# Kernel optimization log

Measured on AMD Instinct MI355X. Metric: run time of the kernel, lower is better.

## Reference

```python
import jax, jax.numpy as jnp
import numpy as np

EPS = 1e-5

def conv1x1(x, w, b):
    # x: [B,C,H,W], w: [O,C], b: [O]
    return jnp.einsum('bchw,oc->bohw', x, w) + b[None, :, None, None]

def bn(x, g, be, m, v):
    inv = g / jnp.sqrt(v + EPS)
    return x * inv[None, :, None, None] + (be - m * inv)[None, :, None, None]

def mrconv4d(x, w, b, g, be, m, v, K):
    B, C, H, W = x.shape
    x_j = jnp.zeros_like(x)
    # torch.cat([x[:,:,-i:,:], x[:,:,:-i,:]], dim=2) == roll by +i along H
    for i in range(K, H, K):
        x_j = jnp.maximum(x_j, x - jnp.roll(x, i, axis=2))
    for i in range(K, W, K):
        x_j = jnp.maximum(x_j, x - jnp.roll(x, i, axis=3))
    y = jnp.concatenate([x, x_j], axis=1)  # [B,2C,H,W]
    y = conv1x1(y, w, b)
    y = bn(y, g, be, m, v)
    return jax.nn.gelu(y, approximate=False)

def setup_inputs() -> dict:
    key = jax.random.key(0)
    ks = jax.random.split(key, 20)
    B, C, H, W = 16, 384, 56, 56
    C2 = 2 * C
    d = {}
    d['x'] = jax.random.normal(ks[0], (B, C, H, W), dtype=jnp.float32)
    d['fc1_w'] = jax.random.normal(ks[1], (C, C), dtype=jnp.float32) * 0.02
    d['fc1_b'] = jax.random.normal(ks[2], (C,), dtype=jnp.float32) * 0.02
    d['fc1_g'] = jax.random.uniform(ks[3], (C,), dtype=jnp.float32) + 0.5
    d['fc1_be'] = jax.random.normal(ks[4], (C,), dtype=jnp.float32) * 0.02
    d['fc1_m'] = jax.random.normal(ks[5], (C,), dtype=jnp.float32) * 0.02
    d['fc1_v'] = jax.random.uniform(ks[6], (C,), dtype=jnp.float32) + 0.5
    d['gc_w'] = jax.random.normal(ks[7], (C2, C2), dtype=jnp.float32) * 0.02
    d['gc_b'] = jax.random.normal(ks[8], (C2,), dtype=jnp.float32) * 0.02
    d['gc_g'] = jax.random.uniform(ks[9], (C2,), dtype=jnp.float32) + 0.5
    d['gc_be'] = jax.random.normal(ks[10], (C2,), dtype=jnp.float32) * 0.02
    d['gc_m'] = jax.random.normal(ks[11], (C2,), dtype=jnp.float32) * 0.02
    d['gc_v'] = jax.random.uniform(ks[12], (C2,), dtype=jnp.float32) + 0.5
    d['fc2_w'] = jax.random.normal(ks[13], (C, C2), dtype=jnp.float32) * 0.02
    d['fc2_b'] = jax.random.normal(ks[14], (C,), dtype=jnp.float32) * 0.02
    d['fc2_g'] = jax.random.uniform(ks[15], (C,), dtype=jnp.float32) + 0.5
    d['fc2_be'] = jax.random.normal(ks[16], (C,), dtype=jnp.float32) * 0.02
    d['fc2_m'] = jax.random.normal(ks[17], (C,), dtype=jnp.float32) * 0.02
    d['fc2_v'] = jax.random.uniform(ks[18], (C,), dtype=jnp.float32) + 0.5
    d['K'] = 2
    return d

def reference(x, fc1_w, fc1_b, fc1_g, fc1_be, fc1_m, fc1_v,
              gc_w, gc_b, gc_g, gc_be, gc_m, gc_v,
              fc2_w, fc2_b, fc2_g, fc2_be, fc2_m, fc2_v, K):
    res = x
    h = bn(conv1x1(x, fc1_w, fc1_b), fc1_g, fc1_be, fc1_m, fc1_v)
    h = mrconv4d(h, gc_w, gc_b, gc_g, gc_be, gc_m, gc_v, K)
    h = bn(conv1x1(h, fc2_w, fc2_b), fc2_g, fc2_be, fc2_m, fc2_v)
    return h + res  # drop_path=0 -> identity
```

## Files before the change

### kernel.cpp

```cpp
#include <hip/hip_runtime.h>

#define P_ 3136
#define NTOT 50176
#define EPSV 1e-5f

typedef __bf16 bf16x8 __attribute__((ext_vector_type(8)));
typedef float f32x4 __attribute__((ext_vector_type(4)));
typedef unsigned short u16x8 __attribute__((ext_vector_type(8)));
typedef unsigned short u16x4 __attribute__((ext_vector_type(4)));

__device__ __forceinline__ unsigned short f2bf(float f) {
    unsigned u = __builtin_bit_cast(unsigned, f);
    unsigned r = u + 0x7fffu + ((u >> 16) & 1u);
    return (unsigned short)(r >> 16);
}
__device__ __forceinline__ float bf2f(unsigned short h) {
    unsigned u = ((unsigned)h) << 16;
    return __builtin_bit_cast(float, u);
}

#if __has_builtin(__builtin_amdgcn_cvt_pk_fp8_f32) && __has_builtin(__builtin_amdgcn_cvt_f32_fp8)
#define FP8_HW 1
#else
#define FP8_HW 0
#endif

__device__ __forceinline__ unsigned f2e4m3_sw(float f) {
    unsigned u = __builtin_bit_cast(unsigned, f);
    unsigned s = (u >> 24) & 0x80u;
    float a = fabsf(f);
    if (a >= 448.f) return s | 0x7Eu;
    if (a < 0.015625f) {
        int m = (int)(a * 512.f + 0.5f);
        return s | (unsigned)m;
    }
    unsigned au = __builtin_bit_cast(unsigned, a);
    unsigned r = au + 0x7FFFFu + ((au >> 20) & 1u);
    unsigned e = (r >> 23) - 120u;
    return s | (e << 3) | ((r >> 20) & 7u);
}
__device__ __forceinline__ float e4m3f_sw(unsigned b) {
    unsigned em = b & 0x7fu;
    float v;
    if (em < 8u) v = (float)em * 0.001953125f;
    else v = __builtin_bit_cast(float, (((em >> 3) + 120u) << 23) | ((em & 7u) << 20));
    return (b & 0x80u) ? -v : v;
}
__device__ __forceinline__ unsigned f2e4m3x4(float v0, float v1, float v2, float v3) {
#if FP8_HW
    unsigned pk = (unsigned)__builtin_amdgcn_cvt_pk_fp8_f32(v0, v1, 0, false);
    pk = (unsigned)__builtin_amdgcn_cvt_pk_fp8_f32(v2, v3, (int)pk, true);
    return pk;
#else
    return f2e4m3_sw(v0) | (f2e4m3_sw(v1) << 8) | (f2e4m3_sw(v2) << 16) | (f2e4m3_sw(v3) << 24);
#endif
}
__device__ __forceinline__ unsigned f2e4m3_1(float v) {
#if FP8_HW
    return (unsigned)__builtin_amdgcn_cvt_pk_fp8_f32(v, 0.f, 0, false) & 0xFFu;
#else
    return f2e4m3_sw(v);
#endif
}
__device__ __forceinline__ float e4m3f(unsigned b) {
#if FP8_HW
    return __builtin_amdgcn_cvt_f32_fp8((int)b, 0);
#else
    return e4m3f_sw(b);
#endif
}

__device__ __forceinline__ float gelu_fast(float x) {
    float x2 = x * x;
    float u2 = x * (1.5957691216f + 0.0713548162f * x2);
    u2 = fminf(u2, 80.0f);
    float e = __expf(u2);
    return x * e * __builtin_amdgcn_rcpf(e + 1.0f);
}
__device__ __forceinline__ void gload16(const void* g, void* l) {
    __builtin_amdgcn_global_load_lds(
        (const __attribute__((address_space(1))) void*)g,
        (__attribute__((address_space(3))) void*)l, 16, 0, 0);
}
__device__ __forceinline__ bf16x8 ldlds(const char* p) {
    return __builtin_bit_cast(bf16x8, *(const u16x8*)p);
}

__global__ __launch_bounds__(256)
void prep_wb(const float* __restrict__ w1, const float* __restrict__ w2,
             const float* __restrict__ w3,
             unsigned short* __restrict__ o1, unsigned char* __restrict__ o2q,
             unsigned char* __restrict__ o3q,
             const float* b1, const float* g1, const float* be1, const float* m1, const float* v1,
             const float* b2, const float* g2, const float* be2, const float* m2, const float* v2,
             const float* b3, const float* g3, const float* be3, const float* m3, const float* v3,
             float* bn1, float* bn2, float* bn3)
{
    int i = blockIdx.x * 256 + threadIdx.x;
    const int n1 = 384 * 384 / 4, n2 = 768 * 768 / 4, n3 = 384 * 768 / 4;
    if (i < n1) {
        float4 f = *(const float4*)(w1 + (size_t)i * 4);
        u16x4 pk = { f2bf(f.x), f2bf(f.y), f2bf(f.z), f2bf(f.w) };
        *(u16x4*)(o1 + (size_t)i * 4) = pk;
    } else if (i < n1 + n2) {
        int j = i - n1;
        float4 f = *(const float4*)(w2 + (size_t)j * 4);
        *(unsigned*)(o2q + (size_t)j * 4) =
            f2e4m3x4(f.x * 32.f, f.y * 32.f, f.z * 32.f, f.w * 32.f);
    } else if (i < n1 + n2 + n3) {
        int j = i - n1 - n2;
        float4 f = *(const float4*)(w3 + (size_t)j * 4);
        *(unsigned*)(o3q + (size_t)j * 4) =
            f2e4m3x4(f.x * 32.f, f.y * 32.f, f.z * 32.f, f.w * 32.f);
    } else {
        int k = i - (n1 + n2 + n3);
        const float *pb, *pg, *pbe, *pm, *pv; float* dst; int o, M; float isc = 1.f;
        if (k < 384)       { pb=b1; pg=g1; pbe=be1; pm=m1; pv=v1; dst=bn1; o=k;      M=384; }
        else if (k < 1152) { pb=b2; pg=g2; pbe=be2; pm=m2; pv=v2; dst=bn2; o=k-384;  M=768; isc = 1.f/32.f; }
        else               { pb=b3; pg=g3; pbe=be3; pm=m3; pv=v3; dst=bn3; o=k-1152; M=384; isc = 1.f/256.f; }
        float inv = pg[o] / sqrtf(pv[o] + EPSV);
        dst[o]     = inv * isc;
        dst[M + o] = (pb[o] - pm[o]) * inv + pbe[o];
    }
}

__global__ __launch_bounds__(256)
void prep_xT(const float* __restrict__ x, unsigned short* __restrict__ xT)
{
    __shared__ float tl[64][65];
    const int t = threadIdx.x;
    const int c0 = blockIdx.x * 64;
    const int p0 = blockIdx.y * 64;
    const int b  = blockIdx.z;
    const float* xb = x + ((size_t)b * 384 + c0) * P_ + p0;
    {
        int c = t >> 2, j0 = (t & 3) * 16;
        #pragma unroll
        for (int j = 0; j < 16; j += 4) {
            float4 f4 = *(const float4*)(xb + (size_t)c * P_ + j0 + j);
            tl[c][j0 + j]     = f4.x; tl[c][j0 + j + 1] = f4.y;
            tl[c][j0 + j + 2] = f4.z; tl[c][j0 + j + 3] = f4.w;
        }
    }
    __syncthreads();
    {
        int p = t >> 2, c1 = (t & 3) * 16;
        unsigned short buf[16];
        #pragma unroll
        for (int j = 0; j < 16; ++j) buf[j] = f2bf(tl[c1 + j][p]);
        unsigned short* dst = xT + ((size_t)b * P_ + p0 + p) * 384 + c0 + c1;
        *(u16x8*)dst       = *(u16x8*)buf;
        *(u16x8*)(dst + 8) = *(u16x8*)(buf + 8);
    }
}

__global__ __launch_bounds__(256, 2)
void gemm1(const unsigned short* __restrict__ W, const unsigned short* __restrict__ In,
           unsigned char* __restrict__ Out, const float* __restrict__ bnp)
{
    constexpr int KD = 384, MDIM = 384, NT = KD / 64, MT = MDIM / 128;
    __shared__ __align__(16) char lds[65536];

    const int t    = threadIdx.x;
    const int lane = t & 63;
    const int wave = t >> 6;
    const int wm = wave >> 1, wn = wave & 1;
    const int fr = lane & 15, fg = lane >> 4;

    const int nwg = gridDim.x;
    int id = blockIdx.x;
    int q = nwg >> 3, r = nwg & 7;
    int xcd = id & 7, pos = id >> 3;
    int wg = (xcd < r ? xcd * (q + 1) : r * (q + 1) + (xcd - r) * q) + pos;
    const int m0 = (wg % MT) * 128;
    const int n0 = (wg / MT) * 128;

    const int pcu  = (((t & 7) ^ ((t >> 3) & 7)) << 3);
    const int srow = t >> 3;
    const unsigned short* pA[4];
    const unsigned short* pB[4];
    #pragma unroll
    for (int i = 0; i < 4; ++i) {
        pA[i] = W  + (size_t)(m0 + i * 32 + srow) * KD + pcu;
        pB[i] = In + (size_t)(n0 + i * 32 + srow) * KD + pcu;
    }
    auto stage = [&](int kt) {
        int kk = kt * 64;
        char* base = lds + (kt & 1) * 32768 + t * 16;
        #pragma unroll
        for (int i = 0; i < 4; ++i) gload16(pA[i] + kk, base + i * 4096);
        #pragma unroll
        for (int i = 0; i < 4; ++i) gload16(pB[i] + kk, base + 16384 + i * 4096);
    };

    const int ko0 = (fg * 16) ^ ((fr & 7) << 4);
    const int ko1 = (64 + fg * 16) ^ ((fr & 7) << 4);
    const int arow = wm * 64 + fr;
    const int brow = wn * 64 + fr;

    f32x4 acc[4][4] = {};

    stage(0);

    for (int kt = 0; kt < NT; ++kt) {
        asm volatile("s_waitcnt vmcnt(0)" ::: "memory");
        __builtin_amdgcn_s_barrier();
        __builtin_amdgcn_sched_barrier(0);
        if (kt + 1 < NT) stage(kt + 1);
        __builtin_amdgcn_sched_barrier(0);

        const char* base = lds + (kt & 1) * 32768;
        bf16x8 afr[4][2], bfr[4][2];
        #pragma unroll
        for (int mf = 0; mf < 4; ++mf) {
            afr[mf][0] = ldlds(base + (arow + mf * 16) * 128 + ko0);
            afr[mf][1] = ldlds(base + (arow + mf * 16) * 128 + ko1);
        }
        #pragma unroll
        for (int nf = 0; nf < 4; ++nf) {
            bfr[nf][0] = ldlds(base + 16384 + (brow + nf * 16) * 128 + ko0);
            bfr[nf][1] = ldlds(base + 16384 + (brow + nf * 16) * 128 + ko1);
        }
        #pragma unroll
        for (int ks = 0; ks < 2; ++ks)
            #pragma unroll
            for (int mf = 0; mf < 4; ++mf)
                #pragma unroll
                for (int nf = 0; nf < 4; ++nf)
                    acc[mf][nf] = __builtin_amdgcn_mfma_f32_16x16x32_bf16(
                        afr[mf][ks], bfr[nf][ks], acc[mf][nf], 0, 0, 0);
    }

    asm volatile("s_waitcnt vmcnt(0)" ::: "memory");
    __builtin_amdgcn_s_barrier();

    unsigned char* eL = (unsigned char*)lds;
    #pragma unroll
    for (int mf = 0; mf < 4; ++mf) {
        const int o_l = wm * 64 + mf * 16 + fg * 4;
        f32x4 inv = *(const f32x4*)(bnp + m0 + o_l);
        f32x4 sh  = *(const f32x4*)(bnp + MDIM + m0 + o_l);
        #pragma unroll
        for (int nf = 0; nf < 4; ++nf) {
            const int col_l = wn * 64 + nf * 16 + fr;
            *(unsigned*)(eL + col_l * 144 + o_l) = f2e4m3x4(
                acc[mf][nf][0] * inv[0] + sh[0],
                acc[mf][nf][1] * inv[1] + sh[1],
                acc[mf][nf][2] * inv[2] + sh[2],
                acc[mf][nf][3] * inv[3] + sh[3]);
        }
    }
    __builtin_amdgcn_s_barrier();
    #pragma unroll
    for (int it = 0; it < 8; ++it) {
        const int idx = it * 256 + t;
        const int col = idx >> 4, seg = idx & 15;
        *(unsigned long long*)(Out + (size_t)(n0 + col) * 768 + m0 + seg * 8) =
            *(const unsigned long long*)(eL + col * 144 + seg * 8);
    }
}

template<int MDIM, int EPI>
__device__ __forceinline__ void gemmq_body(
    const unsigned char* __restrict__ W,
    const unsigned char* __restrict__ In,
    void* __restrict__ OutV,
    const float* __restrict__ bnp,
    const float* __restrict__ res,
    char* lds)
{
    constexpr int NT = 6;
    constexpr int MT = MDIM / 128;

    const int t    = threadIdx.x;
    const int lane = t & 63;
    const int wave = t >> 6;
    const int wm = wave >> 1, wn = wave & 1;
    const int fr = lane & 15, fg = lane >> 4;

    const int nwg = gridDim.x;
    int id = blockIdx.x;
    int q = nwg >> 3, r = nwg & 7;
    int xcd = id & 7, pos = id >> 3;
    int wg = (xcd < r ? xcd * (q + 1) : r * (q + 1) + (xcd - r) * q) + pos;
    const int m0 = (wg % MT) * 128;
    const int n0 = (wg / MT) * 128;

    const int pcu  = (((t & 7) ^ ((t >> 3) & 7)) << 4);
    const int srow = t >> 3;
    const unsigned char* pA[4];
    const unsigned char* pB[4];
    #pragma unroll
    for (int i = 0; i < 4; ++i) {
        pA[i] = W  + (size_t)(m0 + i * 32 + srow) * 768 + pcu;
        pB[i] = In + (size_t)(n0 + i * 32 + srow) * 768 + pcu;
    }
    auto stage = [&](int kt) {
        int kk = kt * 128;
        char* base = lds + (kt & 1) * 32768 + t * 16;
        #pragma unroll
        for (int i = 0; i < 4; ++i) gload16(pA[i] + kk, base + i * 4096);
        #pragma unroll
        for (int i = 0; i < 4; ++i) gload16(pB[i] + kk, base + 16384 + i * 4096);
    };

    const int ko0 = (fg * 16) ^ ((fr & 7) << 4);
    const int ko1 = (64 + fg * 16) ^ ((fr & 7) << 4);
    const int arow = wm * 64 + fr;
    const int brow = wn * 64 + fr;

    f32x4 acc[4][4] = {};

    stage(0);

    for (int kt = 0; kt < NT; ++kt) {
        asm volatile("s_waitcnt vmcnt(0)" ::: "memory");
        __builtin_amdgcn_s_barrier();
        __builtin_amdgcn_sched_barrier(0);
        if (kt + 1 < NT) stage(kt + 1);
        __builtin_amdgcn_sched_barrier(0);

        const char* base = lds + (kt & 1) * 32768;
        ulonglong2 afr[4][2], bfr[4][2];
        #pragma unroll
        for (int mf = 0; mf < 4; ++mf) {
            afr[mf][0] = *(const ulonglong2*)(base + (arow + mf * 16) * 128 + ko0);
            afr[mf][1] = *(const ulonglong2*)(base + (arow + mf * 16) * 128 + ko1);
        }
        #pragma unroll
        for (int nf = 0; nf < 4; ++nf) {
            bfr[nf][0] = *(const ulonglong2*)(base + 16384 + (brow + nf * 16) * 128 + ko0);
            bfr[nf][1] = *(const ulonglong2*)(base + 16384 + (brow + nf * 16) * 128 + ko1);
        }
        #pragma unroll
        for (int rd = 0; rd < 2; ++rd)
            #pragma unroll
            for (int hf = 0; hf < 2; ++hf)
                #pragma unroll
                for (int mf = 0; mf < 4; ++mf)
                    #pragma unroll
                    for (int nf = 0; nf < 4; ++nf)
                        acc[mf][nf] = __builtin_amdgcn_mfma_f32_16x16x32_fp8_fp8(
                            (long)(hf ? afr[mf][rd].y : afr[mf][rd].x),
                            (long)(hf ? bfr[nf][rd].y : bfr[nf][rd].x),
                            acc[mf][nf], 0, 0, 0);
    }

    asm volatile("s_waitcnt vmcnt(0)" ::: "memory");
    __builtin_amdgcn_s_barrier();

    if (EPI == 1) {
        unsigned char* eL = (unsigned char*)lds;
        unsigned char* Out = (unsigned char*)OutV;
        #pragma unroll
        for (int mf = 0; mf < 4; ++mf) {
            const int o_l = wm * 64 + mf * 16 + fg * 4;
            f32x4 inv = *(const f32x4*)(bnp + m0 + o_l);
            f32x4 sh  = *(const f32x4*)(bnp + MDIM + m0 + o_l);
            #pragma unroll
            for (int nf = 0; nf < 4; ++nf) {
                const int col_l = wn * 64 + nf * 16 + fr;
                *(unsigned*)(eL + col_l * 144 + o_l) = f2e4m3x4(
                    gelu_fast(acc[mf][nf][0] * inv[0] + sh[0]) * 8.f,
                    gelu_fast(acc[mf][nf][1] * inv[1] + sh[1]) * 8.f,
                    gelu_fast(acc[mf][nf][2] * inv[2] + sh[2]) * 8.f,
                    gelu_fast(acc[mf][nf][3] * inv[3] + sh[3]) * 8.f);
            }
        }
        __builtin_amdgcn_s_barrier();
        #pragma unroll
        for (int it = 0; it < 8; ++it) {
            const int idx = it * 256 + t;
            const int col = idx >> 4, seg = idx & 15;
            *(unsigned long long*)(Out + (size_t)(n0 + col) * 768 + m0 + seg * 8) =
                *(const unsigned long long*)(eL + col * 144 + seg * 8);
        }
    } else {
        float* eL = (float*)lds;
        float* Out = (float*)OutV;
        #pragma unroll
        for (int mf = 0; mf < 4; ++mf) {
            const int o_l = wm * 64 + mf * 16 + fg * 4;
            f32x4 inv = *(const f32x4*)(bnp + m0 + o_l);
            f32x4 sh  = *(const f32x4*)(bnp + MDIM + m0 + o_l);
            #pragma unroll
            for (int nf = 0; nf < 4; ++nf) {
                const int col_l = wn * 64 + nf * 16 + fr;
                #pragma unroll
                for (int rr = 0; rr < 4; ++rr)
                    eL[(o_l + rr) * 128 + col_l] = acc[mf][nf][rr] * inv[rr] + sh[rr];
            }
        }
        __builtin_amdgcn_s_barrier();
        const int b0 = n0 / P_;
        const int r0 = n0 - b0 * P_;
        #pragma unroll
        for (int g8 = 0; g8 < 8; ++g8) {
            size_t adr[8]; float ev[8], rv[8];
            #pragma unroll
            for (int u = 0; u < 8; ++u) {
                const int idx = (g8 * 8 + u) * 256 + t;
                const int o_i = idx >> 7, col = idx & 127;
                int p = r0 + col;
                const int wrap = p >= P_;
                p -= wrap ? P_ : 0;
                adr[u] = (size_t)(b0 + wrap) * 384 * P_ + (size_t)(m0 + o_i) * P_ + p;
                ev[u]  = eL[o_i * 128 + col];
                rv[u]  = res[adr[u]];
            }
            #pragma unroll
            for (int u = 0; u < 8; ++u)
                Out[adr[u]] = ev[u] + rv[u];
        }
    }
}

__global__ __launch_bounds__(256, 2)
void gemm2q(const unsigned char* __restrict__ W, const unsigned char* __restrict__ In,
            void* __restrict__ OutV, const float* __restrict__ bnp)
{
    __shared__ __align__(16) char lds[65536];
    gemmq_body<768, 1>(W, In, OutV, bnp, nullptr, lds);
}
__global__ __launch_bounds__(256, 2)
void gemm3q(const unsigned char* __restrict__ W, const unsigned char* __restrict__ In,
            void* __restrict__ OutV, const float* __restrict__ bnp,
            const float* __restrict__ res)
{
    __shared__ __align__(16) char lds[65536];
    gemmq_body<384, 2>(W, In, OutV, bnp, res, lds);
}

#define MINSEG (16 * 2 * 56 * 384)
__global__ __launch_bounds__(384)
void mr_min(const unsigned char* __restrict__ y, float* __restrict__ mins)
{
    const int c = threadIdx.x;
    const int q = blockIdx.x;
    const int b = blockIdx.y;
    const unsigned char* yb = y + (size_t)b * P_ * 768;
    float m1e = 3.4e38f, m2e = 3.4e38f, m1o = 3.4e38f, m2o = 3.4e38f;
    if (q < 56) {
        int w = q;
        for (int h = 0; h < 56; h += 2) {
            float v0 = e4m3f(yb[(size_t)(h * 56 + w) * 768 + c]);
            float v1 = e4m3f(yb[(size_t)((h + 1) * 56 + w) * 768 + c]);
            if (v0 < m1e) { m2e = m1e; m1e = v0; } else if (v0 < m2e) m2e = v0;
            if (v1 < m1o) { m2o = m1o; m1o = v1; } else if (v1 < m2o) m2o = v1;
        }
        float* cm1 = mins;
        float* cm2 = mins + MINSEG;
        cm1[((b * 2 + 0) * 56 + w) * 384 + c] = m1e;
        cm1[((b * 2 + 1) * 56 + w) * 384 + c] = m1o;
        cm2[((b * 2 + 0) * 56 + w) * 384 + c] = m2e;
        cm2[((b * 2 + 1) * 56 + w) * 384 + c] = m2o;
    } else {
        int h = q - 56;
        for (int w = 0; w < 56; w += 2) {
            float v0 = e4m3f(yb[(size_t)(h * 56 + w) * 768 + c]);
            float v1 = e4m3f(yb[(size_t)(h * 56 + w + 1) * 768 + c]);
            if (v0 < m1e) { m2e = m1e; m1e = v0; } else if (v0 < m2e) m2e = v0;
            if (v1 < m1o) { m2o = m1o; m1o = v1; } else if (v1 < m2o) m2o = v1;
        }
        float* rm1 = mins + 2 * MINSEG;
        float* rm2 = mins + 3 * MINSEG;
        rm1[((b * 2 + 0) * 56 + h) * 384 + c] = m1e;
        rm1[((b * 2 + 1) * 56 + h) * 384 + c] = m1o;
        rm2[((b * 2 + 0) * 56 + h) * 384 + c] = m2e;
        rm2[((b * 2 + 1) * 56 + h) * 384 + c] = m2o;
    }
}

__global__ __launch_bounds__(384)
void mr_comb(unsigned char* __restrict__ y, const float* __restrict__ mins)
{
    const int c = threadIdx.x;
    const int h = blockIdx.x;
    const int b = blockIdx.y;
    unsigned char* yb = y + (size_t)b * P_ * 768;
    const float* cm1 = mins;
    const float* cm2 = mins + MINSEG;
    const float* rm1 = mins + 2 * MINSEG;
    const float* rm2 = mins + 3 * MINSEG;
    const int parh = h & 1;
    float r1e = rm1[((b * 2 + 0) * 56 + h) * 384 + c];
    float r2e = rm2[((b * 2 + 0) * 56 + h) * 384 + c];
    float r1o = rm1[((b * 2 + 1) * 56 + h) * 384 + c];
    float r2o = rm2[((b * 2 + 1) * 56 + h) * 384 + c];
    #pragma unroll 2
    for (int w = 0; w < 56; ++w) {
        float v  = e4m3f(yb[(size_t)(h * 56 + w) * 768 + c]);
        float c1 = cm1[((b * 2 + parh) * 56 + w) * 384 + c];
        float c2 = cm2[((b * 2 + parh) * 56 + w) * 384 + c];
        float mh = v > c1 ? c1 : c2;
        float rw1 = (w & 1) ? r1o : r1e;
        float rw2 = (w & 1) ? r2o : r2e;
        float mw = v > rw1 ? rw1 : rw2;
        float xj = fmaxf(0.0f, v - fminf(mh, mw));
        yb[(size_t)(h * 56 + w) * 768 + 384 + c] = (unsigned char)f2e4m3_1(xj);
    }
}

extern "C" void kernel_launch(void* const* d_in, const int* in_sizes, int n_in,
                              void* d_out, int out_size, void* d_ws, size_t ws_size,
                              hipStream_t stream)
{
    const float* x      = (const float*)d_in[0];
    const float* fc1_w  = (const float*)d_in[1];
    const float* fc1_b  = (const float*)d_in[2];
    const float* fc1_g  = (const float*)d_in[3];
    const float* fc1_be = (const float*)d_in[4];
    const float* fc1_m  = (const float*)d_in[5];
    const float* fc1_v  = (const float*)d_in[6];
    const float* gc_w   = (const float*)d_in[7];
    const float* gc_b   = (const float*)d_in[8];
    const float* gc_g   = (const float*)d_in[9];
    const float* gc_be  = (const float*)d_in[10];
    const float* gc_m   = (const float*)d_in[11];
    const float* gc_v   = (const float*)d_in[12];
    const float* fc2_w  = (const float*)d_in[13];
    const float* fc2_b  = (const float*)d_in[14];
    const float* fc2_g  = (const float*)d_in[15];
    const float* fc2_be = (const float*)d_in[16];
    const float* fc2_m  = (const float*)d_in[17];
    const float* fc2_v  = (const float*)d_in[18];

    char* ws = (char*)d_ws;
    unsigned char*  y   = (unsigned char*)ws;
    unsigned char*  g   = y + (size_t)NTOT * 768;
    unsigned short* xT  = (unsigned short*)(g + (size_t)NTOT * 768);
    unsigned short* wb1 = xT + (size_t)NTOT * 384;
    unsigned char*  wb2q = (unsigned char*)(wb1 + 384 * 384);
    unsigned char*  wb3q = wb2q + 768 * 768;
    float* bn1 = (float*)(wb3q + 384 * 768);
    float* bn2 = bn1 + 2 * 384;
    float* bn3 = bn2 + 2 * 768;
    float* mins = bn3 + 2 * 384;

    prep_wb<<<1014, 256, 0, stream>>>(fc1_w, gc_w, fc2_w, wb1, wb2q, wb3q,
                                      fc1_b, fc1_g, fc1_be, fc1_m, fc1_v,
                                      gc_b, gc_g, gc_be, gc_m, gc_v,
                                      fc2_b, fc2_g, fc2_be, fc2_m, fc2_v,
                                      bn1, bn2, bn3);
    prep_xT<<<dim3(6, 49, 16), 256, 0, stream>>>(x, xT);

    gemm1<<<dim3(3 * 392), 256, 0, stream>>>(wb1, xT, y, bn1);
    mr_min<<<dim3(112, 16), 384, 0, stream>>>(y, mins);
    mr_comb<<<dim3(56, 16), 384, 0, stream>>>(y, mins);
    gemm2q<<<dim3(6 * 392), 256, 0, stream>>>(wb2q, y, g, bn2);
    gemm3q<<<dim3(3 * 392), 256, 0, stream>>>(wb3q, g, (void*)d_out, bn3, x);
}
```

Before: 190.9 us.

## Enlarge gemm2q tile to 256x256 with 512 threads and 128KB LDS

Splits the shared templated fp8 GEMM body into two dedicated kernels and gives the 768x768 middle GEMM a 256x256 output tile computed by 8 waves (each 128x64) with double-buffered 128KB LDS staging. The aim is to raise arithmetic intensity per loaded byte and cut the number of workgroups, so that redundant global loads of the weight and activation tiles go down. The cost is one workgroup per CU with fewer waves to hide latency, heavier register use from 32 accumulators per thread, and 588 blocks, which may balance unevenly across CUs. gemm3q keeps its previous 128x128 configuration.

```diff
diff --git a/kernel.cpp b/kernel.cpp
--- a/kernel.cpp
+++ b/kernel.cpp
@@ -260,17 +260,129 @@
     }
 }
 
-template<int MDIM, int EPI>
-__device__ __forceinline__ void gemmq_body(
-    const unsigned char* __restrict__ W,
-    const unsigned char* __restrict__ In,
-    void* __restrict__ OutV,
-    const float* __restrict__ bnp,
-    const float* __restrict__ res,
-    char* lds)
+__global__ __launch_bounds__(512, 1)
+void gemm2q(const unsigned char* __restrict__ W,
+            const unsigned char* __restrict__ In,
+            unsigned char* __restrict__ Out,
+            const float* __restrict__ bnp)
 {
     constexpr int NT = 6;
-    constexpr int MT = MDIM / 128;
+    constexpr int MT = 3;
+    __shared__ __align__(16) char lds[131072];
+
+    const int t    = threadIdx.x;
+    const int lane = t & 63;
+    const int wave = t >> 6;
+    const int wm = wave >> 2;
+    const int wn = wave & 3;
+    const int fr = lane & 15, fg = lane >> 4;
+
+    const int nwg = gridDim.x;
+    int id = blockIdx.x;
+    int q = nwg >> 3, r = nwg & 7;
+    int xcd = id & 7, pos = id >> 3;
+    int wg = (xcd < r ? xcd * (q + 1) : r * (q + 1) + (xcd - r) * q) + pos;
+    const int m0 = (wg % MT) * 256;
+    const int n0 = (wg / MT) * 256;
+
+    const int pcu  = (((t & 7) ^ ((t >> 3) & 7)) << 4);
+    const int srow = t >> 3;
+    const unsigned char* pA[4];
+    const unsigned char* pB[4];
+    #pragma unroll
+    for (int i = 0; i < 4; ++i) {
+        pA[i] = W  + (size_t)(m0 + i * 64 + srow) * 768 + pcu;
+        pB[i] = In + (size_t)(n0 + i * 64 + srow) * 768 + pcu;
+    }
+    auto stage = [&](int kt) {
+        int kk = kt * 128;
+        char* base = lds + (kt & 1) * 65536 + t * 16;
+        #pragma unroll
+        for (int i = 0; i < 4; ++i) gload16(pA[i] + kk, base + i * 8192);
+        #pragma unroll
+        for (int i = 0; i < 4; ++i) gload16(pB[i] + kk, base + 32768 + i * 8192);
+    };
+
+    const int ko0 = (fg * 16) ^ ((fr & 7) << 4);
+    const int ko1 = (64 + fg * 16) ^ ((fr & 7) << 4);
+
+    f32x4 acc[8][4] = {};
+
+    stage(0);
+
+    for (int kt = 0; kt < NT; ++kt) {
+        asm volatile("s_waitcnt vmcnt(0)" ::: "memory");
+        __builtin_amdgcn_s_barrier();
+        __builtin_amdgcn_sched_barrier(0);
+        if (kt + 1 < NT) stage(kt + 1);
+        __builtin_amdgcn_sched_barrier(0);
+
+        const char* aB = lds + (kt & 1) * 65536;
+        const char* bB = aB + 32768;
+        #pragma unroll
+        for (int rd = 0; rd < 2; ++rd) {
+            const int ko = rd ? ko1 : ko0;
+            ulonglong2 af[8], bf[4];
+            #pragma unroll
+            for (int mf = 0; mf < 8; ++mf)
+                af[mf] = *(const ulonglong2*)(aB + (wm * 128 + mf * 16 + fr) * 128 + ko);
+            #pragma unroll
+            for (int nf = 0; nf < 4; ++nf)
+                bf[nf] = *(const ulonglong2*)(bB + (wn * 64 + nf * 16 + fr) * 128 + ko);
+            #pragma unroll
+            for (int hf = 0; hf < 2; ++hf)
+                #pragma unroll
+                for (int mf = 0; mf < 8; ++mf)
+                    #pragma unroll
+                    for (int nf = 0; nf < 4; ++nf)
+                        acc[mf][nf] = __builtin_amdgcn_mfma_f32_16x16x32_fp8_fp8(
+                            (long)(hf ? af[mf].y : af[mf].x),
+                            (long)(hf ? bf[nf].y : bf[nf].x),
+                            acc[mf][nf], 0, 0, 0);
+        }
+    }
+
+    asm volatile("s_waitcnt vmcnt(0)" ::: "memory");
+    __builtin_amdgcn_s_barrier();
+
+    unsigned char* eL = (unsigned char*)lds;
+    #pragma unroll
+    for (int mf = 0; mf < 8; ++mf) {
+        const int o_l = wm * 128 + mf * 16 + fg * 4;
+        f32x4 inv = *(const f32x4*)(bnp + m0 + o_l);
+        f32x4 sh  = *(const f32x4*)(bnp + 768 + m0 + o_l);
+        #pragma unroll
+        for (int nf = 0; nf < 4; ++nf) {
+            const int col_l = wn * 64 + nf * 16 + fr;
+            *(unsigned*)(eL + col_l * 272 + o_l) = f2e4m3x4(
+                gelu_fast(acc[mf][nf][0] * inv[0] + sh[0]) * 8.f,
+                gelu_fast(acc[mf][nf][1] * inv[1] + sh[1]) * 8.f,
+                gelu_fast(acc[mf][nf][2] * inv[2] + sh[2]) * 8.f,
+                gelu_fast(acc[mf][nf][3] * inv[3] + sh[3]) * 8.f);
+        }
+    }
+    __builtin_amdgcn_s_barrier();
+    #pragma unroll
+    for (int it = 0; it < 8; ++it) {
+        const int idx = it * 512 + t;
+        const int col = idx >> 4, seg = idx & 15;
+        *(unsigned long long*)(Out + (size_t)(n0 + col) * 768 + m0 + seg * 16) =
+            *(const unsigned long long*)(eL + col * 272 + seg * 16);
+        *(unsigned long long*)(Out + (size_t)(n0 + col) * 768 + m0 + seg * 16 + 8) =
+            *(const unsigned long long*)(eL + col * 272 + seg * 16 + 8);
+    }
+}
+
+__global__ __launch_bounds__(256, 2)
+void gemm3q(const unsigned char* __restrict__ W,
+            const unsigned char* __restrict__ In,
+            float* __restrict__ Out,
+            const float* __restrict__ bnp,
+            const float* __restrict__ res)
+{
+    constexpr int NT = 6;
+    constexpr int MT = 3;
+    __shared__ __align__(16) char lds[65536];
 
     const int t    = threadIdx.x;
     const int lane = t & 63;
@@ -349,86 +461,41 @@
     asm volatile("s_waitcnt vmcnt(0)" ::: "memory");
     __builtin_amdgcn_s_barrier();
 
-    if (EPI == 1) {
-        unsigned char* eL = (unsigned char*)lds;
-        unsigned char* Out = (unsigned char*)OutV;
-        #pragma unroll
-        for (int mf = 0; mf < 4; ++mf) {
-            const int o_l = wm * 64 + mf * 16 + fg * 4;
-            f32x4 inv = *(const f32x4*)(bnp + m0 + o_l);
-            f32x4 sh  = *(const f32x4*)(bnp + MDIM + m0 + o_l);
+    float* eL = (float*)lds;
+    #pragma unroll
+    for (int mf = 0; mf < 4; ++mf) {
+        const int o_l = wm * 64 + mf * 16 + fg * 4;
+        f32x4 inv = *(const f32x4*)(bnp + m0 + o_l);
+        f32x4 sh  = *(const f32x4*)(bnp + 384 + m0 + o_l);
+        #pragma unroll
+        for (int nf = 0; nf < 4; ++nf) {
+            const int col_l = wn * 64 + nf * 16 + fr;
             #pragma unroll
-            for (int nf = 0; nf < 4; ++nf) {
-                const int col_l = wn * 64 + nf * 16 + fr;
-                *(unsigned*)(eL + col_l * 144 + o_l) = f2e4m3x4(
-                    gelu_fast(acc[mf][nf][0] * inv[0] + sh[0]) * 8.f,
-                    gelu_fast(acc[mf][nf][1] * inv[1] + sh[1]) * 8.f,
-                    gelu_fast(acc[mf][nf][2] * inv[2] + sh[2]) * 8.f,
-                    gelu_fast(acc[mf][nf][3] * inv[3] + sh[3]) * 8.f);
-            }
-        }
-        __builtin_amdgcn_s_barrier();
-        #pragma unroll
-        for (int it = 0; it < 8; ++it) {
-            const int idx = it * 256 + t;
-            const int col = idx >> 4, seg = idx & 15;
-            *(unsigned long long*)(Out + (size_t)(n0 + col) * 768 + m0 + seg * 8) =
-                *(const unsigned long long*)(eL + col * 144 + seg * 8);
-        }
-    } else {
-        float* eL = (float*)lds;
-        float* Out = (float*)OutV;
-        #pragma unroll
-        for (int mf = 0; mf < 4; ++mf) {
-            const int o_l = wm * 64 + mf * 16 + fg * 4;
-            f32x4 inv = *(const f32x4*)(bnp + m0 + o_l);
-            f32x4 sh  = *(const f32x4*)(bnp + MDIM + m0 + o_l);
-            #pragma unroll
-            for (int nf = 0; nf < 4; ++nf) {
-                const int col_l = wn * 64 + nf * 16 + fr;
-                #pragma unroll
-                for (int rr = 0; rr < 4; ++rr)
-                    eL[(o_l + rr) * 128 + col_l] = acc[mf][nf][rr] * inv[rr] + sh[rr];
-            }
-        }
-        __builtin_amdgcn_s_barrier();
-        const int b0 = n0 / P_;
-        const int r0 = n0 - b0 * P_;
-        #pragma unroll
-        for (int g8 = 0; g8 < 8; ++g8) {
-            size_t adr[8]; float ev[8], rv[8];
-            #pragma unroll
-            for (int u = 0; u < 8; ++u) {
-                const int idx = (g8 * 8 + u) * 256 + t;
-                const int o_i = idx >> 7, col = idx & 127;
-                int p = r0 + col;
-                const int wrap = p >= P_;
-                p -= wrap ? P_ : 0;
-                adr[u] = (size_t)(b0 + wrap) * 384 * P_ + (size_t)(m0 + o_i) * P_ + p;
-                ev[u]  = eL[o_i * 128 + col];
-                rv[u]  = res[adr[u]];
-            }
-            #pragma unroll
-            for (int u = 0; u < 8; ++u)
-                Out[adr[u]] = ev[u] + rv[u];
-        }
-    }
-}
-
-__global__ __launch_bounds__(256, 2)
-void gemm2q(const unsigned char* __restrict__ W, const unsigned char* __restrict__ In,
-            void* __restrict__ OutV, const float* __restrict__ bnp)
-{
-    __shared__ __align__(16) char lds[65536];
-    gemmq_body<768, 1>(W, In, OutV, bnp, nullptr, lds);
-}
-__global__ __launch_bounds__(256, 2)
-void gemm3q(const unsigned char* __restrict__ W, const unsigned char* __restrict__ In,
-            void* __restrict__ OutV, const float* __restrict__ bnp,
-            const float* __restrict__ res)
-{
-    __shared__ __align__(16) char lds[65536];
-    gemmq_body<384, 2>(W, In, OutV, bnp, res, lds);
+            for (int rr = 0; rr < 4; ++rr)
+                eL[(o_l + rr) * 128 + col_l] = acc[mf][nf][rr] * inv[rr] + sh[rr];
+        }
+    }
+    __builtin_amdgcn_s_barrier();
+    const int b0 = n0 / P_;
+    const int r0 = n0 - b0 * P_;
+    #pragma unroll
+    for (int g8 = 0; g8 < 8; ++g8) {
+        size_t adr[8]; float ev[8], rv[8];
+        #pragma unroll
+        for (int u = 0; u < 8; ++u) {
+            const int idx = (g8 * 8 + u) * 256 + t;
+            const int o_i = idx >> 7, col = idx & 127;
+            int p = r0 + col;
+            const int wrap = p >= P_;
+            p -= wrap ? P_ : 0;
+            adr[u] = (size_t)(b0 + wrap) * 384 * P_ + (size_t)(m0 + o_i) * P_ + p;
+            ev[u]  = eL[o_i * 128 + col];
+            rv[u]  = res[adr[u]];
+        }
+        #pragma unroll
+        for (int u = 0; u < 8; ++u)
+            Out[adr[u]] = ev[u] + rv[u];
+    }
 }
 
 #define MINSEG (16 * 2 * 56 * 384)
@@ -547,6 +614,6 @@
     gemm1<<<dim3(3 * 392), 256, 0, stream>>>(wb1, xT, y, bn1);
     mr_min<<<dim3(112, 16), 384, 0, stream>>>(y, mins);
     mr_comb<<<dim3(56, 16), 384, 0, stream>>>(y, mins);
-    gemm2q<<<dim3(6 * 392), 256, 0, stream>>>(wb2q, y, g, bn2);
-    gemm3q<<<dim3(3 * 392), 256, 0, stream>>>(wb3q, g, (void*)d_out, bn3, x);
-}
+    gemm2q<<<dim3(3 * 196), 512, 0, stream>>>(wb2q, y, g, bn2);
+    gemm3q<<<dim3(3 * 392), 256, 0, stream>>>(wb3q, g, (float*)d_out, bn3, x);
+}
```

After: 217.1 us. 13.7% more time.
